# Kernel tuning notes

Measured on AMD Instinct MI355X. Metric: run time of the kernel, lower is better.

The kernel has to match this reference:

```python
import jax, jax.numpy as jnp
import numpy as np

H, D_IN, E = 8, 512, 512
KD = VD = E // H  # 64
B, N = 16, 1024  # batch, graph_size (== n_query, self-attention)
NEG_INF = -1e30  # stands in for -np.inf; identical post-softmax, NaN-safe


def _uniform(key, shape, stdv):
    return jax.random.uniform(key, shape, jnp.float32, -stdv, stdv)


def setup_inputs() -> dict:
    key = jax.random.key(0)
    kq, km, k1, k2, k3, k4 = jax.random.split(key, 6)
    q = jax.random.normal(kq, (B, N, D_IN), jnp.float32)
    mask = jax.random.bernoulli(km, 0.15, (B, N, N))
    W_query = _uniform(k1, (H, D_IN, KD), 1.0 / np.sqrt(KD))
    W_key = _uniform(k2, (H, D_IN, KD), 1.0 / np.sqrt(KD))
    W_val = _uniform(k3, (H, D_IN, VD), 1.0 / np.sqrt(VD))
    W_out = _uniform(k4, (H, VD, E), 1.0 / np.sqrt(E))
    return {"q": q, "mask": mask, "W_query": W_query, "W_key": W_key,
            "W_val": W_val, "W_out": W_out}


def reference(q, mask, W_query, W_key, W_val, W_out):
    # h = q (self-attention path of the module)
    kd = W_query.shape[-1]
    scale = 1.0 / np.sqrt(kd).astype(np.float32)
    Q = jnp.einsum('bni,hik->hbnk', q, W_query)   # (H,B,N,kd)
    K = jnp.einsum('bgi,hik->hbgk', q, W_key)     # (H,B,G,kd)
    V = jnp.einsum('bgi,hiv->hbgv', q, W_val)     # (H,B,G,vd)
    compat = scale * jnp.einsum('hbnk,hbgk->hbng', Q, K)  # (H,B,N,G)
    m = mask[None]                                 # (1,B,N,G) broadcasts over heads
    compat = jnp.where(m, NEG_INF, compat)
    attn = jax.nn.softmax(compat, axis=-1)
    attn = jnp.where(m, 0.0, attn)
    heads = jnp.einsum('hbng,hbgv->hbnv', attn, V)
    out = jnp.einsum('hbnv,hve->bne', heads, W_out)  # (B,N,E)
    return out
```

## Files before the change

kernel.cpp:

```cpp
#include <hip/hip_runtime.h>
#include <hip/hip_bf16.h>

#define HH 8
#define DIN 512
#define HD 64
#define BB 16
#define NN 1024
#define LOG2E 1.44269504f

typedef float f32x4 __attribute__((ext_vector_type(4)));
typedef short s16x8 __attribute__((ext_vector_type(8)));
typedef unsigned int u32x4 __attribute__((ext_vector_type(4)));
typedef __bf16 bf16x8 __attribute__((ext_vector_type(8)));

__device__ __forceinline__ short f2bf(float f) {
  union { float f; unsigned u; } v; v.f = f;
  unsigned r = v.u + 0x7FFFu + ((v.u >> 16) & 1u);
  return (short)(r >> 16);
}

__device__ __forceinline__ unsigned cvtpk(float lo, float hi) {
  unsigned r;
  asm("v_cvt_pk_bf16_f32 %0, %1, %2" : "=v"(r) : "v"(lo), "v"(hi));
  return r;
}

__device__ __forceinline__ float exp2v(float x) {
  float r;
  asm("v_exp_f32 %0, %1" : "=v"(r) : "v"(x));
  return r;
}

__device__ __forceinline__ f32x4 mfma16(s16x8 a, s16x8 b, f32x4 c) {
  return __builtin_amdgcn_mfma_f32_16x16x32_bf16(
      __builtin_bit_cast(bf16x8, a), __builtin_bit_cast(bf16x8, b), c, 0, 0, 0);
}

#define GLDS16(gsrc, ldst)                                          \
  __builtin_amdgcn_global_load_lds(                                 \
      (const __attribute__((address_space(1))) void*)(gsrc),        \
      (__attribute__((address_space(3))) void*)(ldst), 16, 0, 0)

__global__ void k_detect(const unsigned char* __restrict__ m, int* __restrict__ flag) {
  const int t = threadIdx.x;
  const int nz = (m[4 * t + 1] != 0);
  unsigned long long b = __ballot(nz);
  __shared__ unsigned int anyv;
  if (t == 0) anyv = 0u;
  __syncthreads();
  if ((t & 63) == 0 && b) atomicOr(&anyv, 1u);
  __syncthreads();
  if (t == 0) flag[0] = (int)anyv;
}

__global__ void k_prep(const void* __restrict__ mk, const int* __restrict__ flag,
                       unsigned char* __restrict__ mwords,
                       const float* __restrict__ q, short* __restrict__ qbf,
                       const float* __restrict__ Wq, const float* __restrict__ Wk,
                       const float* __restrict__ Wv, const float* __restrict__ Wo,
                       short* __restrict__ Wt, short* __restrict__ Wot) {
  __shared__ float t[64][65];
  const int blk = blockIdx.x;
  if (blk < 8192) {
    const int i = blk * 256 + threadIdx.x;
    unsigned bits = 0;
    if (flag[0]) {
      const unsigned long long v = ((const unsigned long long*)mk)[i];
#pragma unroll
      for (int j = 0; j < 8; ++j)
        bits |= (((v >> (8 * j)) & 0xFFull) ? 1u : 0u) << j;
    } else {
      const uint4 a = ((const uint4*)mk)[2 * i];
      const uint4 c = ((const uint4*)mk)[2 * i + 1];
      bits = (a.x ? 1u : 0u) | (a.y ? 2u : 0u) | (a.z ? 4u : 0u) | (a.w ? 8u : 0u) |
             (c.x ? 16u : 0u) | (c.y ? 32u : 0u) | (c.z ? 64u : 0u) | (c.w ? 128u : 0u);
    }
    mwords[i] = (unsigned char)bits;
  } else if (blk < 12288) {
    const int i = (blk - 8192) * 256 + threadIdx.x;
    const float4* s4 = (const float4*)q;
    float4 a = s4[2 * i], c = s4[2 * i + 1];
    s16x8 o;
    o[0] = f2bf(a.x); o[1] = f2bf(a.y); o[2] = f2bf(a.z); o[3] = f2bf(a.w);
    o[4] = f2bf(c.x); o[5] = f2bf(c.y); o[6] = f2bf(c.z); o[7] = f2bf(c.w);
    ((s16x8*)qbf)[i] = o;
  } else {
    const int idx = blk - 12288;
    const float* in;
    short* op;
    int N, k0, n0;
    float scale = 1.0f;
    if (idx < 192) {
      const int mat = idx >> 6, rem = idx & 63, head = rem >> 3, kb = rem & 7;
      in = (mat == 0 ? Wq : (mat == 1 ? Wk : Wv)) + head * (DIN * HD);
      op = Wt + (size_t)(mat * 8 + head) * (HD * DIN);
      N = 64; k0 = kb * 64; n0 = 0;
      if (mat == 0) scale = 0.125f * LOG2E;
    } else {
      const int t2 = idx - 192;
      in = Wo; op = Wot;
      N = 512; k0 = (t2 >> 3) * 64; n0 = (t2 & 7) * 64;
    }
    const int tx = threadIdx.x & 63, ty = threadIdx.x >> 6;
#pragma unroll
    for (int i = 0; i < 16; ++i) {
      const int k = ty + i * 4;
      t[k][tx] = in[(size_t)(k0 + k) * N + n0 + tx];
    }
    __syncthreads();
#pragma unroll
    for (int i = 0; i < 16; ++i) {
      const int n = ty + i * 4;
      op[(size_t)(n0 + n) * DIN + k0 + tx] = f2bf(t[tx][n] * scale);
    }
  }
}

template <int MODE>
__global__ __launch_bounds__(256, 2) void k_gemm(
    const short* __restrict__ Abf, const short* __restrict__ Bmat,
    short* __restrict__ Qb, short* __restrict__ Kb, short* __restrict__ VtG,
    float* __restrict__ out) {
  __shared__ short lds[4 * 128 * 64];
  const int tid = threadIdx.x;
  const int m0 = blockIdx.x * 128, n0 = blockIdx.y * 128;
  const int w = tid >> 6, l = tid & 63;
  const int wm = w >> 1, wn = w & 1;
  const int rowf = l & 15, kg = l >> 4;
  const int srow = l >> 3;
  const int cc = (l & 7) ^ srow;
  const bool isV = (MODE == 0) && (n0 >= 1024);

  f32x4 acc[4][4];
#pragma unroll
  for (int i = 0; i < 4; ++i)
#pragma unroll
    for (int j = 0; j < 4; ++j) acc[i][j] = (f32x4){0.f, 0.f, 0.f, 0.f};

  auto issue = [&](int kt, int bsel) {
    short* base = lds + bsel * 16384;
#pragma unroll
    for (int i = 0; i < 4; ++i) {
      const int row = w * 32 + i * 8;
      GLDS16(Abf + ((size_t)(m0 + row + srow) * 512 + kt * 64 + cc * 8),
             base + row * 64);
      GLDS16(Bmat + ((size_t)(n0 + row + srow) * 512 + kt * 64 + cc * 8),
             base + 8192 + row * 64);
    }
  };
  auto compute = [&](int bsel) {
    short* bA = lds + bsel * 16384;
    short* bB = bA + 8192;
#pragma unroll
    for (int kk = 0; kk < 2; ++kk) {
      s16x8 af[4], bf[4];
#pragma unroll
      for (int i = 0; i < 4; ++i) {
        const int arow = wm * 64 + i * 16 + rowf;
        af[i] = *(const s16x8*)&bA[arow * 64 + (((kk * 4 + kg) ^ (arow & 7)) * 8)];
        const int brow = wn * 64 + i * 16 + rowf;
        bf[i] = *(const s16x8*)&bB[brow * 64 + (((kk * 4 + kg) ^ (brow & 7)) * 8)];
      }
      if (isV) {
#pragma unroll
        for (int i = 0; i < 4; ++i)
#pragma unroll
          for (int j = 0; j < 4; ++j) acc[i][j] = mfma16(bf[j], af[i], acc[i][j]);
      } else {
#pragma unroll
        for (int i = 0; i < 4; ++i)
#pragma unroll
          for (int j = 0; j < 4; ++j) acc[i][j] = mfma16(af[i], bf[j], acc[i][j]);
      }
    }
  };

  issue(0, 0);
  issue(1, 1);
#pragma unroll 1
  for (int kt = 0; kt < 7; ++kt) {
    asm volatile("s_waitcnt vmcnt(8)" ::: "memory");
    __builtin_amdgcn_sched_barrier(0);
    __builtin_amdgcn_s_barrier();
    compute(kt & 1);
    __builtin_amdgcn_s_barrier();
    __builtin_amdgcn_sched_barrier(0);
    if (kt + 2 < 8) issue(kt + 2, kt & 1);
  }
  asm volatile("s_waitcnt vmcnt(0)" ::: "memory");
  __builtin_amdgcn_sched_barrier(0);
  __builtin_amdgcn_s_barrier();
  compute(1);

  if (MODE == 1) {
#pragma unroll
    for (int i = 0; i < 4; ++i)
#pragma unroll
      for (int j = 0; j < 4; ++j)
#pragma unroll
        for (int r = 0; r < 4; ++r) {
          const int m = m0 + wm * 64 + i * 16 + kg * 4 + r;
          const int n = n0 + wn * 64 + j * 16 + rowf;
          out[(size_t)m * DIN + n] = acc[i][j][r];
        }
  } else if (isV) {
    const int bconst = m0 >> 10;
#pragma unroll
    for (int i = 0; i < 4; ++i)
#pragma unroll
      for (int j = 0; j < 4; ++j)
#pragma unroll
        for (int r = 0; r < 4; ++r) {
          const int ng = n0 + wn * 64 + j * 16 + kg * 4 + r;
          const int head = (ng >> 6) & 7, d = ng & 63;
          const int m = m0 + wm * 64 + i * 16 + rowf;
          const int seq = m & 1023;
          VtG[((size_t)(head * BB + bconst) * HD + d) * NN + seq] = f2bf(acc[i][j][r]);
        }
  } else {
#pragma unroll
    for (int i = 0; i < 4; ++i)
#pragma unroll
      for (int j = 0; j < 4; ++j)
#pragma unroll
        for (int r = 0; r < 4; ++r) {
          const int m = m0 + wm * 64 + i * 16 + kg * 4 + r;
          const int ng = n0 + wn * 64 + j * 16 + rowf;
          const int mat = ng >> 9, head = (ng >> 6) & 7, d = ng & 63;
          short* Ob = (mat == 0 ? Qb : Kb) + head * (BB * NN * HD);
          Ob[(size_t)m * HD + d] = f2bf(acc[i][j][r]);
        }
  }
}

__global__ __launch_bounds__(512, 4) void k_attn(
    const short* __restrict__ Qb, const short* __restrict__ Kb, const short* __restrict__ VtG,
    const unsigned int* __restrict__ mw, short* __restrict__ heads) {
  __shared__ short smem[2 * 8192];
  const int tid = threadIdx.x;
  const int w = tid >> 6, l = tid & 63, rowf = l & 15, kg = l >> 4;
  const int r7 = rowf & 7;
  const int lin = blockIdx.x;
  const int gi = (lin >> 3) + ((lin & 7) << 6);
  const int qblk = gi & 3, bh = gi >> 2;
  const int b = bh & 15, h = bh >> 4;
  const int hb = (h * BB + b) * NN;
  const short* Qp = Qb + (size_t)hb * HD;
  const short* Kp = Kb + (size_t)hb * HD;
  const short* Vtp = VtG + (size_t)(h * BB + b) * HD * NN;
  const int wq = qblk * 256 + w * 32;

  s16x8 bQ[2][2];
#pragma unroll
  for (int qi = 0; qi < 2; ++qi)
#pragma unroll
    for (int kk = 0; kk < 2; ++kk)
      bQ[qi][kk] = *(const s16x8*)&Qp[(wq + qi * 16 + rowf) * HD + kk * 32 + kg * 8];

  const f32x4 cW = (f32x4){-24.f, -24.f, -24.f, -24.f};
  f32x4 accO[2][4], accSum[2];
#pragma unroll
  for (int qi = 0; qi < 2; ++qi) {
    accSum[qi] = (f32x4){0.f, 0.f, 0.f, 0.f};
#pragma unroll
    for (int vj = 0; vj < 4; ++vj) accO[qi][vj] = (f32x4){0.f, 0.f, 0.f, 0.f};
  }
  s16x8 aOnes;
#pragma unroll
  for (int jj = 0; jj < 8; ++jj) aOnes[jj] = (short)0x3F80;

  const int Rs = w * 8 + (l >> 3), cp = l & 7;
  const int im = Rs >> 4, ii = Rs & 15;
  const int keyRs = (im >> 1) * 32 + ((ii >> 2) & 3) * 8 + (im & 1) * 4 + (ii & 3);
  const short* srcK = Kp + keyRs * HD + ((cp ^ (Rs & 7)) * 8);
  const short* srcV = Vtp + (size_t)Rs * NN + ((cp ^ (Rs & 7)) * 8);

  auto issueT = [&](int t) {
    short* base = smem + (t & 1) * 8192;
    GLDS16(srcK + (size_t)t * 64 * HD, base + w * 512);
    GLDS16(srcV + t * 64, base + 4096 + w * 512);
  };

  const unsigned int* mrow0 = mw + (size_t)(b * NN + wq + rowf) * 32;

  issueT(0);
#pragma unroll 1
  for (int kt = 0; kt < NN / 64; ++kt) {
    asm volatile("s_waitcnt vmcnt(0)" ::: "memory");
    __builtin_amdgcn_sched_barrier(0);
    __builtin_amdgcn_s_barrier();
    if (kt + 1 < NN / 64) issueT(kt + 1);
    short* bK = smem + (kt & 1) * 8192;
    short* bV = bK + 4096;

    f32x4 accS[2][4];
    __builtin_amdgcn_s_setprio(1);
#pragma unroll
    for (int m = 0; m < 4; ++m) {
      const int R = m * 16 + rowf;
      s16x8 a0 = *(const s16x8*)&bK[R * 64 + ((kg ^ r7) * 8)];
      s16x8 a1 = *(const s16x8*)&bK[R * 64 + (((4 + kg) ^ r7) * 8)];
      accS[0][m] = mfma16(a0, bQ[0][0], cW);
      accS[0][m] = mfma16(a1, bQ[0][1], accS[0][m]);
      accS[1][m] = mfma16(a0, bQ[1][0], cW);
      accS[1][m] = mfma16(a1, bQ[1][1], accS[1][m]);
    }
    __builtin_amdgcn_s_setprio(0);

#pragma unroll
    for (int qi = 0; qi < 2; ++qi) {
      const uint2 mv = *(const uint2*)(mrow0 + qi * 512 + kt * 2);
      const unsigned u0 = mv.x >> (kg * 8);
      const unsigned u1 = mv.y >> (kg * 8);
      u32x4 pw[2];
#pragma unroll
      for (int half = 0; half < 2; ++half) {
        const unsigned u = half ? u1 : u0;
        u32x4 wd;
#pragma unroll
        for (int t = 0; t < 4; ++t) {
          const int j0 = 2 * t, j1 = 2 * t + 1;
          const float e0 = ((u >> j0) & 1u) ? 0.f
                           : exp2v(accS[qi][half * 2 + (j0 >> 2)][j0 & 3]);
          const float e1 = ((u >> j1) & 1u) ? 0.f
                           : exp2v(accS[qi][half * 2 + (j1 >> 2)][j1 & 3]);
          wd[t] = cvtpk(e0, e1);
        }
        pw[half] = wd;
      }
      __builtin_amdgcn_s_setprio(1);
#pragma unroll
      for (int kk = 0; kk < 2; ++kk) {
        const s16x8 pa = __builtin_bit_cast(s16x8, pw[kk]);
        accSum[qi] = mfma16(aOnes, pa, accSum[qi]);
#pragma unroll
        for (int vj = 0; vj < 4; ++vj) {
          const int d = vj * 16 + rowf;
          s16x8 aV = *(const s16x8*)&bV[d * 64 + (((kk * 4 + kg) ^ r7) * 8)];
          accO[qi][vj] = mfma16(aV, pa, accO[qi][vj]);
        }
      }
      __builtin_amdgcn_s_setprio(0);
    }
  }

  __syncthreads();
  short* tb = smem + w * 2048;
  {
    const float rc0 = 1.0f / accSum[0][0], rc1 = 1.0f / accSum[1][0];
#pragma unroll
    for (int qi = 0; qi < 2; ++qi) {
      const float rc = qi ? rc1 : rc0;
      const int row = qi * 16 + rowf;
#pragma unroll
      for (int vj = 0; vj < 4; ++vj)
#pragma unroll
        for (int r = 0; r < 4; ++r) {
          const int col = vj * 16 + kg * 4 + r;
          tb[row * 64 + (((col >> 3) ^ (row & 7)) * 8) + (col & 7)] =
              f2bf(accO[qi][vj][r] * rc);
        }
    }
  }
#pragma unroll
  for (int it = 0; it < 4; ++it) {
    const int ql = (l >> 3) + it * 8, oct = l & 7;
    s16x8 v = *(const s16x8*)&tb[ql * 64 + ((oct ^ (ql & 7)) * 8)];
    *(s16x8*)&heads[((size_t)(b * NN + wq + ql) * HH + h) * HD + oct * 8] = v;
  }
}

extern "C" void kernel_launch(void* const* d_in, const int* in_sizes, int n_in,
                              void* d_out, int out_size, void* d_ws, size_t ws_size,
                              hipStream_t stream) {
  if (n_in < 6) return;
  const float* q  = (const float*)d_in[0];
  const void*  mk = d_in[1];
  const float* Wq = (const float*)d_in[2];
  const float* Wk = (const float*)d_in[3];
  const float* Wv = (const float*)d_in[4];
  const float* Wo = (const float*)d_in[5];
  float* out = (float*)d_out;

  char* ws = (char*)d_ws;
  size_t o = 0;
  auto alloc = [&](size_t sz) { char* p = ws + o; o = (o + sz + 255) & ~(size_t)255; return p; };
  int*           flag   = (int*)alloc(4);
  unsigned char* mwords = (unsigned char*)alloc((size_t)BB * NN * NN / 8);
  short* qbf   = (short*)alloc((size_t)BB * NN * DIN * 2);
  short* Wt    = (short*)alloc((size_t)3 * HH * HD * DIN * 2);
  short* Wot   = (short*)alloc((size_t)DIN * DIN * 2);
  short* Qbuf  = (short*)alloc((size_t)HH * BB * NN * HD * 2);
  short* Kbuf  = (short*)alloc((size_t)HH * BB * NN * HD * 2);
  short* VtBuf = (short*)alloc((size_t)HH * BB * HD * NN * 2);
  short* heads = (short*)alloc((size_t)BB * NN * HH * HD * 2);
  if (o > ws_size) return;

  k_detect<<<1, 256, 0, stream>>>((const unsigned char*)mk, flag);
  k_prep<<<12544, 256, 0, stream>>>(mk, flag, mwords, q, qbf, Wq, Wk, Wv, Wo, Wt, Wot);
  k_gemm<0><<<dim3(BB * NN / 128, 12), 256, 0, stream>>>(
      qbf, Wt, Qbuf, Kbuf, VtBuf, nullptr);
  k_attn<<<dim3(512), 512, 0, stream>>>(Qbuf, Kbuf, VtBuf,
                                        (const unsigned int*)mwords, heads);
  k_gemm<1><<<dim3(BB * NN / 128, 4), 256, 0, stream>>>(
      heads, Wot, nullptr, nullptr, nullptr, out);
}
```

Measured before the change: 119.9 us.

## Split attention key range across two wave groups with LDS reduction

The attention block grows from 512 to 1024 threads. Two groups of 8 waves each process half of the key sequence (512 keys, 8 tiles) for the same query rows, each with its own double-buffered LDS K/V staging. Partial output accumulators and row sums are then reduced through LDS before normalisation and the store. This doubles the waves available per block to hide latency and halves the serial loop length, at the cost of a larger LDS footprint, an extra reduction step, and possibly lower occupancy from the 1024-thread launch bound.

```diff
diff --git a/kernel.cpp b/kernel.cpp
--- a/kernel.cpp
+++ b/kernel.cpp
@@ -233,13 +233,15 @@
   }
 }
 
-__global__ __launch_bounds__(512, 4) void k_attn(
+__global__ __launch_bounds__(1024) void k_attn(
     const short* __restrict__ Qb, const short* __restrict__ Kb, const short* __restrict__ VtG,
     const unsigned int* __restrict__ mw, short* __restrict__ heads) {
-  __shared__ short smem[2 * 8192];
+  __shared__ short smem[32768];
+  __shared__ float ssumLds[8][2][16];
   const int tid = threadIdx.x;
   const int w = tid >> 6, l = tid & 63, rowf = l & 15, kg = l >> 4;
   const int r7 = rowf & 7;
+  const int g = w >> 3, p8 = w & 7;
   const int lin = blockIdx.x;
   const int gi = (lin >> 3) + ((lin & 7) << 6);
   const int qblk = gi & 3, bh = gi >> 2;
@@ -248,7 +250,7 @@
   const short* Qp = Qb + (size_t)hb * HD;
   const short* Kp = Kb + (size_t)hb * HD;
   const short* Vtp = VtG + (size_t)(h * BB + b) * HD * NN;
-  const int wq = qblk * 256 + w * 32;
+  const int wq = qblk * 256 + p8 * 32;
 
   s16x8 bQ[2][2];
 #pragma unroll
@@ -269,37 +271,39 @@
 #pragma unroll
   for (int jj = 0; jj < 8; ++jj) aOnes[jj] = (short)0x3F80;
 
-  const int Rs = w * 8 + (l >> 3), cp = l & 7;
-  const int im = Rs >> 4, ii = Rs & 15;
-  const int keyRs = (im >> 1) * 32 + ((ii >> 2) & 3) * 8 + (im & 1) * 4 + (ii & 3);
-  const short* srcK = Kp + keyRs * HD + ((cp ^ (Rs & 7)) * 8);
-  const short* srcV = Vtp + (size_t)Rs * NN + ((cp ^ (Rs & 7)) * 8);
+  const int lr = l >> 3, cp = l & 7;
+  const int R = p8 * 8 + lr;
+  const int im = R >> 4, ii = R & 15;
+  const int keyR = (im >> 1) * 32 + ((ii >> 2) & 3) * 8 + (im & 1) * 4 + (ii & 3);
+  const short* srcK = Kp + (size_t)(g * 512 + keyR) * HD + ((cp ^ (R & 7)) * 8);
+  const short* srcV = Vtp + (size_t)R * NN + g * 512 + ((cp ^ (R & 7)) * 8);
+  short* sbase = smem + g * 16384;
 
   auto issueT = [&](int t) {
-    short* base = smem + (t & 1) * 8192;
-    GLDS16(srcK + (size_t)t * 64 * HD, base + w * 512);
-    GLDS16(srcV + t * 64, base + 4096 + w * 512);
+    short* base = sbase + (t & 1) * 8192;
+    GLDS16(srcK + (size_t)t * 64 * HD, base + (p8 * 8) * 64);
+    GLDS16(srcV + t * 64, base + 4096 + (p8 * 8) * 64);
   };
 
-  const unsigned int* mrow0 = mw + (size_t)(b * NN + wq + rowf) * 32;
+  const unsigned int* mrow0 = mw + (size_t)(b * NN + wq + rowf) * 32 + g * 16;
 
   issueT(0);
 #pragma unroll 1
-  for (int kt = 0; kt < NN / 64; ++kt) {
+  for (int kt = 0; kt < 8; ++kt) {
     asm volatile("s_waitcnt vmcnt(0)" ::: "memory");
     __builtin_amdgcn_sched_barrier(0);
     __builtin_amdgcn_s_barrier();
-    if (kt + 1 < NN / 64) issueT(kt + 1);
-    short* bK = smem + (kt & 1) * 8192;
+    if (kt + 1 < 8) issueT(kt + 1);
+    short* bK = sbase + (kt & 1) * 8192;
     short* bV = bK + 4096;
 
     f32x4 accS[2][4];
     __builtin_amdgcn_s_setprio(1);
 #pragma unroll
     for (int m = 0; m < 4; ++m) {
-      const int R = m * 16 + rowf;
-      s16x8 a0 = *(const s16x8*)&bK[R * 64 + ((kg ^ r7) * 8)];
-      s16x8 a1 = *(const s16x8*)&bK[R * 64 + (((4 + kg) ^ r7) * 8)];
+      const int Rr = m * 16 + rowf;
+      s16x8 a0 = *(const s16x8*)&bK[Rr * 64 + ((kg ^ r7) * 8)];
+      s16x8 a1 = *(const s16x8*)&bK[Rr * 64 + (((4 + kg) ^ r7) * 8)];
       accS[0][m] = mfma16(a0, bQ[0][0], cW);
       accS[0][m] = mfma16(a1, bQ[0][1], accS[0][m]);
       accS[1][m] = mfma16(a0, bQ[1][0], cW);
@@ -345,8 +349,35 @@
   }
 
   __syncthreads();
-  short* tb = smem + w * 2048;
-  {
+  float* cO = (float*)smem;
+  if (g == 0) {
+#pragma unroll
+    for (int qi = 0; qi < 2; ++qi) {
+      const int q = qi * 16 + rowf;
+#pragma unroll
+      for (int vj = 0; vj < 4; ++vj) {
+        const int c = (vj * 4 + kg) ^ (q & 15);
+        *(f32x4*)&cO[p8 * 2048 + q * 64 + c * 4] = accO[qi][vj];
+      }
+    }
+    ssumLds[p8][0][rowf] = accSum[0][0];
+    ssumLds[p8][1][rowf] = accSum[1][0];
+  }
+  __syncthreads();
+  if (g == 1) {
+#pragma unroll
+    for (int qi = 0; qi < 2; ++qi) {
+      const int q = qi * 16 + rowf;
+#pragma unroll
+      for (int vj = 0; vj < 4; ++vj) {
+        const int c = (vj * 4 + kg) ^ (q & 15);
+        accO[qi][vj] += *(const f32x4*)&cO[p8 * 2048 + q * 64 + c * 4];
+      }
+    }
+    accSum[0][0] += ssumLds[p8][0][rowf];
+    accSum[1][0] += ssumLds[p8][1][rowf];
+
+    short* tb = (short*)&cO[p8 * 2048];
     const float rc0 = 1.0f / accSum[0][0], rc1 = 1.0f / accSum[1][0];
 #pragma unroll
     for (int qi = 0; qi < 2; ++qi) {
@@ -361,12 +392,12 @@
               f2bf(accO[qi][vj][r] * rc);
         }
     }
-  }
-#pragma unroll
-  for (int it = 0; it < 4; ++it) {
-    const int ql = (l >> 3) + it * 8, oct = l & 7;
-    s16x8 v = *(const s16x8*)&tb[ql * 64 + ((oct ^ (ql & 7)) * 8)];
-    *(s16x8*)&heads[((size_t)(b * NN + wq + ql) * HH + h) * HD + oct * 8] = v;
+#pragma unroll
+    for (int it = 0; it < 4; ++it) {
+      const int ql = (l >> 3) + it * 8, oct = l & 7;
+      s16x8 v = *(const s16x8*)&tb[ql * 64 + ((oct ^ (ql & 7)) * 8)];
+      *(s16x8*)&heads[((size_t)(b * NN + wq + ql) * HH + h) * HD + oct * 8] = v;
+    }
   }
 }
 
@@ -400,8 +431,8 @@
   k_prep<<<12544, 256, 0, stream>>>(mk, flag, mwords, q, qbf, Wq, Wk, Wv, Wo, Wt, Wot);
   k_gemm<0><<<dim3(BB * NN / 128, 12), 256, 0, stream>>>(
       qbf, Wt, Qbuf, Kbuf, VtBuf, nullptr);
-  k_attn<<<dim3(512), 512, 0, stream>>>(Qbuf, Kbuf, VtBuf,
-                                        (const unsigned int*)mwords, heads);
+  k_attn<<<dim3(512), 1024, 0, stream>>>(Qbuf, Kbuf, VtBuf,
+                                         (const unsigned int*)mwords, heads);
   k_gemm<1><<<dim3(BB * NN / 128, 4), 256, 0, stream>>>(
       heads, Wot, nullptr, nullptr, nullptr, out);
 }
```

New measurement: 126.1 us. +5.2%, slower.

## Double key tile to 128 per barrier and share V fragments across query halves

Applied to the files above, without the earlier changes.

The attention loop now stages 128 keys per iteration (two 64-key sub-tiles) in a doubled shared-memory buffer, which halves the number of barrier and wait points. The PV stage is reordered so each V fragment read from LDS feeds both query sub-blocks, which halves LDS reads of V. The occupancy hint in launch_bounds is dropped. LDS use doubles to 64 KB per block and register pressure from keeping pw for both query halves live may rise, which could reduce occupancy.

```diff
diff --git a/kernel.cpp b/kernel.cpp
--- a/kernel.cpp
+++ b/kernel.cpp
@@ -233,10 +233,10 @@
   }
 }
 
-__global__ __launch_bounds__(512, 4) void k_attn(
+__global__ __launch_bounds__(512) void k_attn(
     const short* __restrict__ Qb, const short* __restrict__ Kb, const short* __restrict__ VtG,
     const unsigned int* __restrict__ mw, short* __restrict__ heads) {
-  __shared__ short smem[2 * 8192];
+  __shared__ short smem[2 * 16384];
   const int tid = threadIdx.x;
   const int w = tid >> 6, l = tid & 63, rowf = l & 15, kg = l >> 4;
   const int r7 = rowf & 7;
@@ -269,75 +269,89 @@
 #pragma unroll
   for (int jj = 0; jj < 8; ++jj) aOnes[jj] = (short)0x3F80;
 
-  const int Rs = w * 8 + (l >> 3), cp = l & 7;
-  const int im = Rs >> 4, ii = Rs & 15;
-  const int keyRs = (im >> 1) * 32 + ((ii >> 2) & 3) * 8 + (im & 1) * 4 + (ii & 3);
-  const short* srcK = Kp + keyRs * HD + ((cp ^ (Rs & 7)) * 8);
-  const short* srcV = Vtp + (size_t)Rs * NN + ((cp ^ (Rs & 7)) * 8);
+  const int lr = l >> 3, cp = l & 7;
+  const int R = w * 8 + lr;
+  const int im = R >> 4, ii = R & 15;
+  const int keyR = (im >> 1) * 32 + ((ii >> 2) & 3) * 8 + (im & 1) * 4 + (ii & 3);
+  const short* srcK = Kp + (size_t)keyR * HD + ((cp ^ (R & 7)) * 8);
+  const short* srcV = Vtp + (size_t)R * NN + ((cp ^ (R & 7)) * 8);
 
   auto issueT = [&](int t) {
-    short* base = smem + (t & 1) * 8192;
-    GLDS16(srcK + (size_t)t * 64 * HD, base + w * 512);
-    GLDS16(srcV + t * 64, base + 4096 + w * 512);
+    short* base = smem + (t & 1) * 16384;
+#pragma unroll
+    for (int s = 0; s < 2; ++s) {
+      const int key0 = t * 128 + s * 64;
+      GLDS16(srcK + (size_t)key0 * HD, base + s * 4096 + (w * 8) * 64);
+      GLDS16(srcV + key0, base + 8192 + s * 4096 + (w * 8) * 64);
+    }
   };
 
   const unsigned int* mrow0 = mw + (size_t)(b * NN + wq + rowf) * 32;
 
   issueT(0);
 #pragma unroll 1
-  for (int kt = 0; kt < NN / 64; ++kt) {
+  for (int kt = 0; kt < 8; ++kt) {
     asm volatile("s_waitcnt vmcnt(0)" ::: "memory");
     __builtin_amdgcn_sched_barrier(0);
     __builtin_amdgcn_s_barrier();
-    if (kt + 1 < NN / 64) issueT(kt + 1);
-    short* bK = smem + (kt & 1) * 8192;
-    short* bV = bK + 4096;
-
-    f32x4 accS[2][4];
-    __builtin_amdgcn_s_setprio(1);
-#pragma unroll
-    for (int m = 0; m < 4; ++m) {
-      const int R = m * 16 + rowf;
-      s16x8 a0 = *(const s16x8*)&bK[R * 64 + ((kg ^ r7) * 8)];
-      s16x8 a1 = *(const s16x8*)&bK[R * 64 + (((4 + kg) ^ r7) * 8)];
-      accS[0][m] = mfma16(a0, bQ[0][0], cW);
-      accS[0][m] = mfma16(a1, bQ[0][1], accS[0][m]);
-      accS[1][m] = mfma16(a0, bQ[1][0], cW);
-      accS[1][m] = mfma16(a1, bQ[1][1], accS[1][m]);
-    }
-    __builtin_amdgcn_s_setprio(0);
-
-#pragma unroll
-    for (int qi = 0; qi < 2; ++qi) {
-      const uint2 mv = *(const uint2*)(mrow0 + qi * 512 + kt * 2);
-      const unsigned u0 = mv.x >> (kg * 8);
-      const unsigned u1 = mv.y >> (kg * 8);
-      u32x4 pw[2];
-#pragma unroll
-      for (int half = 0; half < 2; ++half) {
-        const unsigned u = half ? u1 : u0;
-        u32x4 wd;
-#pragma unroll
-        for (int t = 0; t < 4; ++t) {
-          const int j0 = 2 * t, j1 = 2 * t + 1;
-          const float e0 = ((u >> j0) & 1u) ? 0.f
-                           : exp2v(accS[qi][half * 2 + (j0 >> 2)][j0 & 3]);
-          const float e1 = ((u >> j1) & 1u) ? 0.f
-                           : exp2v(accS[qi][half * 2 + (j1 >> 2)][j1 & 3]);
-          wd[t] = cvtpk(e0, e1);
-        }
-        pw[half] = wd;
+    if (kt + 1 < 8) issueT(kt + 1);
+    short* base = smem + (kt & 1) * 16384;
+
+#pragma unroll
+    for (int s = 0; s < 2; ++s) {
+      short* bK = base + s * 4096;
+      short* bV = base + 8192 + s * 4096;
+
+      f32x4 accS[2][4];
+      __builtin_amdgcn_s_setprio(1);
+#pragma unroll
+      for (int m = 0; m < 4; ++m) {
+        const int Rr = m * 16 + rowf;
+        s16x8 a0 = *(const s16x8*)&bK[Rr * 64 + ((kg ^ r7) * 8)];
+        s16x8 a1 = *(const s16x8*)&bK[Rr * 64 + (((4 + kg) ^ r7) * 8)];
+        accS[0][m] = mfma16(a0, bQ[0][0], cW);
+        accS[0][m] = mfma16(a1, bQ[0][1], accS[0][m]);
+        accS[1][m] = mfma16(a0, bQ[1][0], cW);
+        accS[1][m] = mfma16(a1, bQ[1][1], accS[1][m]);
       }
+      __builtin_amdgcn_s_setprio(0);
+
+      u32x4 pw[2][2];
+#pragma unroll
+      for (int qi = 0; qi < 2; ++qi) {
+        const uint2 mv = *(const uint2*)(mrow0 + qi * 512 + (kt * 2 + s) * 2);
+        const unsigned u0 = mv.x >> (kg * 8);
+        const unsigned u1 = mv.y >> (kg * 8);
+#pragma unroll
+        for (int half = 0; half < 2; ++half) {
+          const unsigned u = half ? u1 : u0;
+          u32x4 wd;
+#pragma unroll
+          for (int t2 = 0; t2 < 4; ++t2) {
+            const int j0 = 2 * t2, j1 = 2 * t2 + 1;
+            const float e0 = ((u >> j0) & 1u) ? 0.f
+                             : exp2v(accS[qi][half * 2 + (j0 >> 2)][j0 & 3]);
+            const float e1 = ((u >> j1) & 1u) ? 0.f
+                             : exp2v(accS[qi][half * 2 + (j1 >> 2)][j1 & 3]);
+            wd[t2] = cvtpk(e0, e1);
+          }
+          pw[qi][half] = wd;
+        }
+      }
+
       __builtin_amdgcn_s_setprio(1);
 #pragma unroll
       for (int kk = 0; kk < 2; ++kk) {
-        const s16x8 pa = __builtin_bit_cast(s16x8, pw[kk]);
-        accSum[qi] = mfma16(aOnes, pa, accSum[qi]);
+        const s16x8 pa0 = __builtin_bit_cast(s16x8, pw[0][kk]);
+        const s16x8 pa1 = __builtin_bit_cast(s16x8, pw[1][kk]);
+        accSum[0] = mfma16(aOnes, pa0, accSum[0]);
+        accSum[1] = mfma16(aOnes, pa1, accSum[1]);
 #pragma unroll
         for (int vj = 0; vj < 4; ++vj) {
           const int d = vj * 16 + rowf;
           s16x8 aV = *(const s16x8*)&bV[d * 64 + (((kk * 4 + kg) ^ r7) * 8)];
-          accO[qi][vj] = mfma16(aV, pa, accO[qi][vj]);
+          accO[0][vj] = mfma16(aV, pa0, accO[0][vj]);
+          accO[1][vj] = mfma16(aV, pa1, accO[1][vj]);
         }
       }
       __builtin_amdgcn_s_setprio(0);
```

After: 135.4 us. +13.0%, slower.
